# Optimization experiments

Hardware: AMD Instinct MI355X
Metric: run time of the kernel (lower is better)

Reference implementation:

```python
import jax, jax.numpy as jnp
import numpy as np

N, E = 20000, 320000
IN_CH, HID, NPRED = 64, 512, 12
NUM_GCN = 3   # num_gcn_layers=4 -> 1 + (4-2) layers
NUM_RNN = 2
BN_EPS = 1e-5


def setup_inputs() -> dict:
    key = jax.random.key(0)
    ks = jax.random.split(key, 16)
    s = 0.05  # init scale to keep activations sane
    return {
        "x": jax.random.normal(ks[0], (N, IN_CH), jnp.float32),
        "edge_index": jax.random.randint(ks[1], (2, E), 0, N, jnp.int32),
        "edge_weight": jax.random.uniform(ks[2], (E,), jnp.float32),
        "gcn0_W": jax.random.normal(ks[3], (IN_CH, HID), jnp.float32) * s,
        "gcn0_b": jnp.zeros((HID,), jnp.float32),
        "gcn_W": jax.random.normal(ks[4], (NUM_GCN - 1, HID, HID), jnp.float32) * s,
        "gcn_b": jnp.zeros((NUM_GCN - 1, HID), jnp.float32),
        "bn_gamma": jnp.ones((NUM_GCN, HID), jnp.float32),
        "bn_beta": jnp.zeros((NUM_GCN, HID), jnp.float32),
        "w_ih": jax.random.normal(ks[5], (NUM_RNN, HID, 4 * HID), jnp.float32) * s,
        "w_hh": jax.random.normal(ks[6], (NUM_RNN, HID, 4 * HID), jnp.float32) * s,
        "w_ch": jax.random.normal(ks[7], (NUM_RNN, HID, 3 * HID), jnp.float32) * s,
        "lstm_b": jnp.zeros((NUM_RNN, 4 * HID), jnp.float32),
        "out_W": jax.random.normal(ks[8], (HID, NPRED), jnp.float32) * s,
        "out_b": jnp.zeros((NPRED,), jnp.float32),
    }


def _gcn(x, W, b, src, dst, ew, n):
    h = x @ W                                   # [N, out]
    msg = ew[:, None] * h[src]                  # [E, out]
    return jax.ops.segment_sum(msg, dst, num_segments=n) + b


def _bn_relu(x, gamma, beta):
    mu = jnp.mean(x, axis=0)
    var = jnp.var(x, axis=0)
    return jax.nn.relu((x - mu) * jax.lax.rsqrt(var + BN_EPS) * gamma + beta)


def _peephole_cell(inp, h, c, Wih, Whh, Wch, b):
    H = h.shape[1]
    gates = inp @ Wih + h @ Whh + b             # [N, 4H]
    i_g, f_g, g_g, o_g = jnp.split(gates, 4, axis=1)
    g_g = g_g + c @ Wch[:, :H]
    i_g = jax.nn.sigmoid(i_g)
    f_g = jax.nn.sigmoid(f_g + c @ Wch[:, H:2 * H])
    g_g = jnp.tanh(g_g)
    cy = f_g * c + i_g * g_g
    o_g = o_g + cy @ Wch[:, 2 * H:]
    hy = jax.nn.sigmoid(o_g) * jnp.tanh(cy)
    return hy, cy


def reference(x, edge_index, edge_weight, gcn0_W, gcn0_b, gcn_W, gcn_b,
              bn_gamma, bn_beta, w_ih, w_hh, w_ch, lstm_b, out_W, out_b):
    src, dst = edge_index[0], edge_index[1]
    n = x.shape[0]
    # GCN stack: conv -> batchnorm (train-mode stats) -> relu (dropout=0)
    h = _gcn(x, gcn0_W, gcn0_b, src, dst, edge_weight, n)
    h = _bn_relu(h, bn_gamma[0], bn_beta[0])
    for i in range(NUM_GCN - 1):
        h = _gcn(h, gcn_W[i], gcn_b[i], src, dst, edge_weight, n)
        h = _bn_relu(h, bn_gamma[i + 1], bn_beta[i + 1])
    # seq_len == 1 after unsqueeze; cells chained sharing (h_t, c_t)
    h_t = jnp.zeros((n, HID), h.dtype)
    c_t = jnp.zeros((n, HID), h.dtype)
    for l in range(NUM_RNN):
        h_t, c_t = _peephole_cell(h, h_t, c_t, w_ih[l], w_hh[l], w_ch[l], lstm_b[l])
    out = h_t @ out_W + out_b                   # [N, num_predictions]
    return jnp.squeeze(out)
```

## Files before the change

kernel.cpp:

```cpp
#include <hip/hip_runtime.h>
#include <cstddef>

#define N_NODES 20000
#define N_EDGES 320000
#define IN_CH   64
#define HID     512
#define G4      2048
#define BN_EPS  1e-5f
#define F_OFF   0
#define G_OFF   512
#define I_OFF   1024
#define O_OFF   1536

typedef __attribute__((ext_vector_type(8))) __bf16 bf16x8;
typedef __attribute__((ext_vector_type(4))) float f32x4;

__device__ __forceinline__ float sigmoidf_(float x) {
  return 1.0f / (1.0f + expf(-x));
}

__device__ __forceinline__ unsigned short f2b(float f) {
  unsigned int u = __float_as_uint(f);
  u += 0x7FFFu + ((u >> 16) & 1u);
  return (unsigned short)(u >> 16);
}
__device__ __forceinline__ float b2f(unsigned short u) {
  return __uint_as_float(((unsigned int)u) << 16);
}

__device__ __forceinline__ void gld_lds16(const unsigned short* g, unsigned short* l) {
  __builtin_amdgcn_global_load_lds(
      (const __attribute__((address_space(1))) unsigned int*)(const void*)g,
      (__attribute__((address_space(3))) unsigned int*)(void*)l, 16, 0, 0);
}

__global__ __launch_bounds__(256) void zero_k(float* __restrict__ p, size_t n) {
  size_t i = ((size_t)blockIdx.x * 256 + threadIdx.x) * 4;
  if (i + 3 < n) {
    *(float4*)&p[i] = make_float4(0.f, 0.f, 0.f, 0.f);
  } else {
    for (; i < n; i++) p[i] = 0.f;
  }
}

struct TcvtDesc { const float* W; unsigned short* Wt; int K, NC, ldw, ldo; };
struct TcvtBatch { TcvtDesc d[18]; };

__global__ void tcvtb_k(TcvtBatch batch) {
  const TcvtDesc dd = batch.d[blockIdx.z];
  __shared__ float tile[32][33];
  const int n0 = blockIdx.x * 32, k0 = blockIdx.y * 32;
  if (n0 >= dd.NC || k0 >= dd.K) return;
  const int tx = threadIdx.x, ty = threadIdx.y;
  #pragma unroll
  for (int i = 0; i < 32; i += 8) {
    int k = k0 + ty + i, n = n0 + tx;
    tile[ty + i][tx] = (k < dd.K && n < dd.NC) ? dd.W[(size_t)k * dd.ldw + n] : 0.f;
  }
  __syncthreads();
  #pragma unroll
  for (int i = 0; i < 32; i += 8) {
    int n = n0 + ty + i, k = k0 + tx;
    if (n < dd.NC && k < dd.K) dd.Wt[(size_t)n * dd.ldo + k] = f2b(tile[tx][ty + i]);
  }
}

__global__ __launch_bounds__(256) void hist_k(const int* __restrict__ dst,
                                              int* __restrict__ counts) {
  int e = blockIdx.x * 256 + threadIdx.x;
  if (e < N_EDGES) atomicAdd(&counts[dst[e]], 1);
}

__global__ __launch_bounds__(1024) void scan_k(const int* __restrict__ counts,
                                               int* __restrict__ offsets,
                                               int* __restrict__ pos, int n) {
  __shared__ int tmp[1024];
  __shared__ int carry_s;
  const int tid = threadIdx.x;
  if (tid == 0) carry_s = 0;
  __syncthreads();
  for (int base = 0; base < n; base += 1024) {
    int i = base + tid;
    int v = (i < n) ? counts[i] : 0;
    tmp[tid] = v;
    __syncthreads();
    #pragma unroll
    for (int off = 1; off < 1024; off <<= 1) {
      int t = (tid >= off) ? tmp[tid - off] : 0;
      __syncthreads();
      tmp[tid] += t;
      __syncthreads();
    }
    if (i < n) {
      int excl = carry_s + tmp[tid] - v;
      offsets[i] = excl;
      pos[i] = excl;
    }
    __syncthreads();
    if (tid == 1023) carry_s += tmp[1023];
    __syncthreads();
  }
  if (tid == 0) offsets[n] = carry_s;
}

__global__ __launch_bounds__(256) void fill_k(
    const int* __restrict__ src, const int* __restrict__ dst,
    const float* __restrict__ ew, int* __restrict__ pos,
    int* __restrict__ s_s, float* __restrict__ w_s) {
  int e = blockIdx.x * 256 + threadIdx.x;
  if (e >= N_EDGES) return;
  int p = atomicAdd(&pos[dst[e]], 1);
  s_s[p] = src[e];
  w_s[p] = ew[e];
}

__global__ __launch_bounds__(64) void gather64_k(
    const float* __restrict__ x, const int* __restrict__ offsets,
    const int* __restrict__ s_s, const float* __restrict__ w_s,
    unsigned short* __restrict__ xg) {
  const int sub = threadIdx.x >> 4;
  const int cg  = threadIdx.x & 15;
  const int n   = blockIdx.x * 4 + sub;
  const int beg = offsets[n], end = offsets[n + 1];
  float4 acc = make_float4(0.f, 0.f, 0.f, 0.f);
  int i = beg;
  for (; i + 3 < end; i += 4) {
    const int   s0 = s_s[i],     s1 = s_s[i + 1];
    const int   s2 = s_s[i + 2], s3 = s_s[i + 3];
    const float w0 = w_s[i],     w1 = w_s[i + 1];
    const float w2 = w_s[i + 2], w3 = w_s[i + 3];
    const float4 v0 = *(const float4*)&x[(size_t)s0 * IN_CH + cg * 4];
    const float4 v1 = *(const float4*)&x[(size_t)s1 * IN_CH + cg * 4];
    const float4 v2 = *(const float4*)&x[(size_t)s2 * IN_CH + cg * 4];
    const float4 v3 = *(const float4*)&x[(size_t)s3 * IN_CH + cg * 4];
    acc.x = fmaf(w0, v0.x, acc.x); acc.y = fmaf(w0, v0.y, acc.y);
    acc.z = fmaf(w0, v0.z, acc.z); acc.w = fmaf(w0, v0.w, acc.w);
    acc.x = fmaf(w1, v1.x, acc.x); acc.y = fmaf(w1, v1.y, acc.y);
    acc.z = fmaf(w1, v1.z, acc.z); acc.w = fmaf(w1, v1.w, acc.w);
    acc.x = fmaf(w2, v2.x, acc.x); acc.y = fmaf(w2, v2.y, acc.y);
    acc.z = fmaf(w2, v2.z, acc.z); acc.w = fmaf(w2, v2.w, acc.w);
    acc.x = fmaf(w3, v3.x, acc.x); acc.y = fmaf(w3, v3.y, acc.y);
    acc.z = fmaf(w3, v3.z, acc.z); acc.w = fmaf(w3, v3.w, acc.w);
  }
  for (; i < end; i++) {
    const int   s = s_s[i];
    const float w = w_s[i];
    const float4 v = *(const float4*)&x[(size_t)s * IN_CH + cg * 4];
    acc.x = fmaf(w, v.x, acc.x);
    acc.y = fmaf(w, v.y, acc.y);
    acc.z = fmaf(w, v.z, acc.z);
    acc.w = fmaf(w, v.w, acc.w);
  }
  ushort4 o; o.x = f2b(acc.x); o.y = f2b(acc.y); o.z = f2b(acc.z); o.w = f2b(acc.w);
  *(ushort4*)&xg[(size_t)n * IN_CH + cg * 4] = o;
}

__global__ __launch_bounds__(128) void gather_k(
    const unsigned short* __restrict__ XW, const int* __restrict__ offsets,
    const int* __restrict__ s_s, const float* __restrict__ w_s,
    unsigned short* __restrict__ H) {
  const int n = blockIdx.x;
  const int t = threadIdx.x;
  const int beg = offsets[n], end = offsets[n + 1];
  float4 acc = make_float4(0.f, 0.f, 0.f, 0.f);
  int i = beg;
  for (; i + 3 < end; i += 4) {
    const int   s0 = s_s[i],     s1 = s_s[i + 1];
    const int   s2 = s_s[i + 2], s3 = s_s[i + 3];
    const float w0 = w_s[i],     w1 = w_s[i + 1];
    const float w2 = w_s[i + 2], w3 = w_s[i + 3];
    const ushort4 v0 = *(const ushort4*)&XW[(size_t)s0 * HID + t * 4];
    const ushort4 v1 = *(const ushort4*)&XW[(size_t)s1 * HID + t * 4];
    const ushort4 v2 = *(const ushort4*)&XW[(size_t)s2 * HID + t * 4];
    const ushort4 v3 = *(const ushort4*)&XW[(size_t)s3 * HID + t * 4];
    acc.x = fmaf(w0, b2f(v0.x), acc.x); acc.y = fmaf(w0, b2f(v0.y), acc.y);
    acc.z = fmaf(w0, b2f(v0.z), acc.z); acc.w = fmaf(w0, b2f(v0.w), acc.w);
    acc.x = fmaf(w1, b2f(v1.x), acc.x); acc.y = fmaf(w1, b2f(v1.y), acc.y);
    acc.z = fmaf(w1, b2f(v1.z), acc.z); acc.w = fmaf(w1, b2f(v1.w), acc.w);
    acc.x = fmaf(w2, b2f(v2.x), acc.x); acc.y = fmaf(w2, b2f(v2.y), acc.y);
    acc.z = fmaf(w2, b2f(v2.z), acc.z); acc.w = fmaf(w2, b2f(v2.w), acc.w);
    acc.x = fmaf(w3, b2f(v3.x), acc.x); acc.y = fmaf(w3, b2f(v3.y), acc.y);
    acc.z = fmaf(w3, b2f(v3.z), acc.z); acc.w = fmaf(w3, b2f(v3.w), acc.w);
  }
  for (; i < end; i++) {
    const int   s = s_s[i];
    const float w = w_s[i];
    const ushort4 v = *(const ushort4*)&XW[(size_t)s * HID + t * 4];
    acc.x = fmaf(w, b2f(v.x), acc.x);
    acc.y = fmaf(w, b2f(v.y), acc.y);
    acc.z = fmaf(w, b2f(v.z), acc.z);
    acc.w = fmaf(w, b2f(v.w), acc.w);
  }
  ushort4 o; o.x = f2b(acc.x); o.y = f2b(acc.y); o.z = f2b(acc.z); o.w = f2b(acc.w);
  *(ushort4*)&H[(size_t)n * HID + t * 4] = o;
}

__global__ __launch_bounds__(256) void bn_stats_k(
    const unsigned short* __restrict__ H, float* __restrict__ stats, int N)
{
  const int tx = threadIdx.x & 63;
  const int ty = threadIdx.x >> 6;
  const int col = blockIdx.x * 64 + tx;
  float s1 = 0.f, s2 = 0.f;
  for (int r = blockIdx.y * 4 + ty; r < N; r += gridDim.y * 4) {
    float v = b2f(H[(size_t)r * HID + col]);
    s1 += v; s2 += v * v;
  }
  __shared__ float red[2][4][64];
  red[0][ty][tx] = s1;
  red[1][ty][tx] = s2;
  __syncthreads();
  if (ty == 0) {
    s1 = red[0][0][tx] + red[0][1][tx] + red[0][2][tx] + red[0][3][tx];
    s2 = red[1][0][tx] + red[1][1][tx] + red[1][2][tx] + red[1][3][tx];
    atomicAdd(&stats[col], s1);
    atomicAdd(&stats[HID + col], s2);
  }
}

__global__ __launch_bounds__(256) void bn_apply_k(
    const unsigned short* __restrict__ H, const float* __restrict__ stats,
    const float* __restrict__ gamma, const float* __restrict__ beta,
    unsigned short* __restrict__ out, int N)
{
  size_t gid = (size_t)blockIdx.x * 256 + threadIdx.x;
  size_t idx = gid * 4;
  if (idx >= (size_t)N * HID) return;
  int col = (int)(idx & (HID - 1));
  const ushort4 v = *(const ushort4*)&H[idx];
  float r[4] = {b2f(v.x), b2f(v.y), b2f(v.z), b2f(v.w)};
  ushort4 o;
  unsigned short* op = &o.x;
  #pragma unroll
  for (int i = 0; i < 4; i++) {
    int c = col + i;
    float mean = stats[c] * (1.0f / N);
    float var  = stats[HID + c] * (1.0f / N) - mean * mean;
    float scale = gamma[c] / sqrtf(var + BN_EPS);
    float shift = beta[c] - mean * scale;
    op[i] = f2b(fmaxf(fmaf(r[i], scale, shift), 0.0f));
  }
  *(ushort4*)&out[idx] = o;
}

template<int BM, int BN>
__global__ __launch_bounds__(256) void gemm_bf16_k(
    const unsigned short* __restrict__ A, int lda,
    const unsigned short* __restrict__ A2, int lda2, int ksplit,
    const unsigned short* __restrict__ Bt,
    float* __restrict__ C, unsigned short* __restrict__ C16,
    const float* __restrict__ bias,
    int M, int K, int Ksmall, int NC, int ldc, int acc, int ntc,
    int nrowb, int ncolb)
{
  const int b   = blockIdx.x;
  const int xcd = b & 7;
  const int j   = b >> 3;
  const int col_b = j % ncolb;
  const int row_b = (j / ncolb) * 8 + xcd;
  if (row_b >= nrowb) return;

  constexpr int MI  = 2;
  constexpr int ASZ = BM * 64;
  constexpr int BSZ = BN * 64;
  __shared__ unsigned short As[2 * ASZ];
  __shared__ unsigned short Bs[2 * BSZ];
  const int row0 = row_b * BM;
  const int col0 = col_b * BN;
  const int Kthis = (col0 < 1024) ? K : Ksmall;
  const int t    = threadIdx.x;
  const int lane = t & 63;
  const int w    = t >> 6;
  const int wro  = (BN == 128) ? (w >> 1) * 32 : w * 32;
  const int wco  = (BN == 128) ? (w & 1) * 64 : 0;
  const int q    = lane >> 4;
  const int l16  = lane & 15;

  f32x4 accr[MI][4] = {};

  auto stage = [&](int buf, int k0) {
    unsigned short* Ad = As + buf * ASZ;
    unsigned short* Bd = Bs + buf * BSZ;
    #pragma unroll
    for (int i = 0; i < BM / 32; i++) {
      int s  = t + i * 256;
      int r  = s >> 3, cq = s & 7;
      int kq = (cq - r) & 7;
      int gr = row0 + r; if (gr > M - 1) gr = M - 1;
      int kk = k0 + kq * 8;
      const unsigned short* bp = (kk < ksplit) ? A : A2;
      size_t off = (kk < ksplit) ? ((size_t)gr * lda + kk)
                                 : ((size_t)gr * lda2 + (kk - ksplit));
      gld_lds16(bp + off, Ad + (size_t)s * 8);
    }
    #pragma unroll
    for (int i = 0; i < BN / 32; i++) {
      int s  = t + i * 256;
      int r  = s >> 3, cq = s & 7;
      int kq = (cq - r) & 7;
      gld_lds16(Bt + (size_t)(col0 + r) * K + k0 + kq * 8, Bd + (size_t)s * 8);
    }
  };

  stage(0, 0);
  int cur = 0;
  for (int k0 = 0; k0 < Kthis; k0 += 64) {
    __syncthreads();
    if (k0 + 64 < Kthis) stage(cur ^ 1, k0 + 64);

    const unsigned short* Ac = As + cur * ASZ;
    const unsigned short* Bc = Bs + cur * BSZ;
    #pragma unroll
    for (int ks = 0; ks < 2; ks++) {
      bf16x8 af[MI], bfr[4];
      #pragma unroll
      for (int mi = 0; mi < MI; mi++) {
        int r = wro + mi * 16 + l16;
        int slot = (ks * 4 + q + r) & 7;
        af[mi] = *(const bf16x8*)&Ac[r * 64 + slot * 8];
      }
      #pragma unroll
      for (int ni = 0; ni < 4; ni++) {
        int r = wco + ni * 16 + l16;
        int slot = (ks * 4 + q + r) & 7;
        bfr[ni] = *(const bf16x8*)&Bc[r * 64 + slot * 8];
      }
      #pragma unroll
      for (int mi = 0; mi < MI; mi++)
        #pragma unroll
        for (int ni = 0; ni < 4; ni++)
          accr[mi][ni] = __builtin_amdgcn_mfma_f32_16x16x32_bf16(
              af[mi], bfr[ni], accr[mi][ni], 0, 0, 0);
    }
    cur ^= 1;
  }

  #pragma unroll
  for (int mi = 0; mi < MI; mi++) {
    #pragma unroll
    for (int ni = 0; ni < 4; ni++) {
      int col = col0 + wco + ni * 16 + l16;
      #pragma unroll
      for (int r = 0; r < 4; r++) {
        int row = row0 + wro + mi * 16 + q * 4 + r;
        if (row < M) {
          float v = accr[mi][ni][r];
          if (C16) {
            C16[(size_t)row * ldc + col] = f2b(v);
          } else {
            float* cp = &C[(size_t)row * ldc + col];
            if (acc)       *cp += v;
            else if (bias) *cp  = v + bias[col];
            else if (ntc)  __builtin_nontemporal_store(v, cp);
            else           *cp  = v;
          }
        }
      }
    }
  }
}

__global__ __launch_bounds__(256) void cell1_k(
    const float* __restrict__ gates, const float* __restrict__ lb,
    const float* __restrict__ cin,
    float* __restrict__ cout, unsigned short* __restrict__ cout16, int ld16,
    int rows, int hasC)
{
  size_t gid = (size_t)blockIdx.x * 256 + threadIdx.x;
  if (gid >= (size_t)rows * HID) return;
  size_t row = gid >> 9;
  int    col = (int)(gid & (HID - 1));
  const float* g = &gates[row * G4];
  float ig = sigmoidf_(__builtin_nontemporal_load(&g[I_OFF + col]) + lb[col]);
  float gg = tanhf(__builtin_nontemporal_load(&g[G_OFF + col]) + lb[2 * HID + col]);
  float c;
  if (hasC) {
    float fg = sigmoidf_(__builtin_nontemporal_load(&g[F_OFF + col]) + lb[HID + col]);
    c = fg * cin[gid] + ig * gg;
  } else {
    c = ig * gg;
  }
  cout[gid] = c;
  cout16[row * ld16 + col] = f2b(c);
}

__global__ __launch_bounds__(256) void cell2_k(
    const float* __restrict__ gates, const float* __restrict__ obuf,
    const float* __restrict__ lb, const float* __restrict__ cy,
    unsigned short* __restrict__ hy16, int ld16, int rows)
{
  size_t gid = (size_t)blockIdx.x * 256 + threadIdx.x;
  if (gid >= (size_t)rows * HID) return;
  size_t row = gid >> 9;
  int    col = (int)(gid & (HID - 1));
  float ov = __builtin_nontemporal_load(&gates[row * G4 + O_OFF + col]);
  float og = sigmoidf_(ov + obuf[gid] + lb[3 * HID + col]);
  float h = og * tanhf(cy[gid]);
  hy16[row * ld16 + col] = f2b(h);
}

__global__ __launch_bounds__(256) void cellout_k(
    const float* __restrict__ gates, const float* __restrict__ obuf,
    const float* __restrict__ lb, const float* __restrict__ cy,
    const float* __restrict__ W, const float* __restrict__ b,
    float* __restrict__ out, int rows)
{
  int wave = (int)(((size_t)blockIdx.x * 256 + threadIdx.x) >> 6);
  int lane = threadIdx.x & 63;
  if (wave >= rows) return;
  const float* g  = &gates[(size_t)wave * G4 + O_OFF];
  const float* ob = &obuf[(size_t)wave * HID];
  const float* cr = &cy[(size_t)wave * HID];
  float hy[8];
  #pragma unroll
  for (int j = 0; j < 8; j++) {
    int k = lane + j * 64;
    float og = sigmoidf_(__builtin_nontemporal_load(&g[k]) + ob[k] + lb[3 * HID + k]);
    hy[j] = og * tanhf(cr[k]);
  }
  float acc[12] = {};
  #pragma unroll
  for (int j = 0; j < 8; j++) {
    int k = lane + j * 64;
    const float* wr = &W[k * 12];
    #pragma unroll
    for (int p = 0; p < 12; p++) acc[p] = fmaf(hy[j], wr[p], acc[p]);
  }
  #pragma unroll
  for (int p = 0; p < 12; p++) {
    float v = acc[p];
    #pragma unroll
    for (int off = 32; off > 0; off >>= 1) v += __shfl_down(v, off);
    if (lane == 0) out[(size_t)wave * 12 + p] = v + b[p];
  }
}

extern "C" void kernel_launch(void* const* d_in, const int* in_sizes, int n_in,
                              void* d_out, int out_size, void* d_ws, size_t ws_size,
                              hipStream_t stream) {
  const float* x     = (const float*)d_in[0];
  const int*   ei    = (const int*)d_in[1];
  const float* ew    = (const float*)d_in[2];
  const float* gcn0W = (const float*)d_in[3];
  const float* gcnW  = (const float*)d_in[5];
  const float* gamma = (const float*)d_in[7];
  const float* beta  = (const float*)d_in[8];
  const float* wih   = (const float*)d_in[9];
  const float* whh   = (const float*)d_in[10];
  const float* wch   = (const float*)d_in[11];
  const float* lstmb = (const float*)d_in[12];
  const float* outW  = (const float*)d_in[13];
  const float* outb  = (const float*)d_in[14];
  float* out = (float*)d_out;

  const int* src = ei;
  const int* dst = ei + N_EDGES;

  const int CH = (ws_size >= (size_t)215000000) ? 10000 : 5000;
  const int NCHUNK = N_NODES / CH;

  const size_t NH = (size_t)N_NODES * HID;
  float* ws = (float*)d_ws;
  float* gates = ws;
  float* bufH  = gates + (size_t)CH * G4;
  unsigned short* hbA16 = (unsigned short*)(bufH + NH);
  unsigned short* hbB16 = hbA16 + NH;
  unsigned short* x16   = hbB16 + NH;
  unsigned short* g0t   = x16 + (size_t)N_NODES * IN_CH;
  unsigned short* g1t   = g0t   + 512 * 64;
  unsigned short* g2t   = g1t   + 512 * 512;
  unsigned short* wih0t = g2t   + 512 * 512;
  unsigned short* wcat3 = wih0t + (size_t)1536 * 512;
  unsigned short* wch0ot= wcat3 + (size_t)2048 * 1536;
  unsigned short* wch1ot= wch0ot + 512 * 512;
  unsigned short* wend  = wch1ot + 512 * 512;
  unsigned short *a16, *tail16;
  if (CH == 5000) {
    a16  = hbB16;
    tail16 = wend;
  } else {
    a16  = wend;
    tail16 = a16 + (size_t)CH * 1024;
  }
  float* stats = (float*)tail16;
  int*   csr   = (int*)(stats + 3072);
  int*   counts  = csr;
  int*   offsets = csr + 20032;
  int*   cpos    = csr + 40064;
  int*   s_s     = csr + 60096;
  float* w_s     = (float*)(csr + 380096);

  unsigned short* bufH16 = (unsigned short*)bufH;
  float* cbuf = bufH;
  float* obuf = bufH + (size_t)CH * HID;

  const dim3 blk(256);
  auto gemm128 = [&](const unsigned short* A, int lda,
                     const unsigned short* A2, int lda2, int ksplit,
                     const unsigned short* Bt, float* C, unsigned short* C16,
                     const float* bias, int M, int K, int Ksmall, int NC, int ldc,
                     int acc) {
    int nrowb = (M + 63) / 64;
    int ncolb = NC / 128;
    int nblocks = 8 * ((nrowb + 7) / 8) * ncolb;
    hipLaunchKernelGGL((gemm_bf16_k<64, 128>), dim3(nblocks), blk, 0, stream,
                       A, lda, A2, lda2, ksplit, Bt, C, C16, bias,
                       M, K, Ksmall, NC, ldc, acc, 1, nrowb, ncolb);
  };
  auto gemm64 = [&](const unsigned short* A, int lda,
                    const unsigned short* Bt, float* C, unsigned short* C16,
                    const float* bias, int M, int K, int NC, int ldc, int acc) {
    int nrowb = (M + 127) / 128;
    int ncolb = NC / 64;
    int nblocks = 8 * ((nrowb + 7) / 8) * ncolb;
    hipLaunchKernelGGL((gemm_bf16_k<128, 64>), dim3(nblocks), blk, 0, stream,
                       A, lda, A, lda, K, Bt, C, C16, bias,
                       M, K, K, NC, ldc, acc, 0, nrowb, ncolb);
  };
  auto zero = [&](float* p, size_t n) {
    hipLaunchKernelGGL(zero_k, dim3((unsigned)((n / 4 + 255) / 256)), blk, 0, stream, p, n);
  };

  const float* wih1 = wih + (size_t)HID * G4;
  const float* whh1 = whh + (size_t)HID * G4;
  const float* wch1 = wch + (size_t)HID * 3 * HID;
  {
    TcvtBatch tb;
    int n = 0;
    auto add = [&](const float* W, unsigned short* Wt, int K, int NC, int ldw, int ldo) {
      tb.d[n++] = TcvtDesc{W, Wt, K, NC, ldw, ldo};
    };
    add(gcn0W, g0t, IN_CH, HID, HID, IN_CH);
    add(gcnW,                     g1t, HID, HID, HID, HID);
    add(gcnW + (size_t)HID * HID, g2t, HID, HID, HID, HID);
    add(wih + 2 * HID, wih0t,                      HID, HID, G4, HID);
    add(wih,           wih0t + (size_t)512 * 512,  HID, HID, G4, HID);
    add(wih + 3 * HID, wih0t + (size_t)1024 * 512, HID, HID, G4, HID);
    add(wih1 + HID,     wcat3 + (size_t)F_OFF * 1536,        HID, HID, G4, 1536);
    add(whh1 + HID,     wcat3 + (size_t)F_OFF * 1536 + 512,  HID, HID, G4, 1536);
    add(wch1 + HID,     wcat3 + (size_t)F_OFF * 1536 + 1024, HID, HID, 3 * HID, 1536);
    add(wih1 + 2 * HID, wcat3 + (size_t)G_OFF * 1536,        HID, HID, G4, 1536);
    add(whh1 + 2 * HID, wcat3 + (size_t)G_OFF * 1536 + 512,  HID, HID, G4, 1536);
    add(wch1,           wcat3 + (size_t)G_OFF * 1536 + 1024, HID, HID, 3 * HID, 1536);
    add(wih1,           wcat3 + (size_t)I_OFF * 1536,        HID, HID, G4, 1536);
    add(whh1,           wcat3 + (size_t)I_OFF * 1536 + 512,  HID, HID, G4, 1536);
    add(wih1 + 3 * HID, wcat3 + (size_t)O_OFF * 1536,        HID, HID, G4, 1536);
    add(whh1 + 3 * HID, wcat3 + (size_t)O_OFF * 1536 + 512,  HID, HID, G4, 1536);
    add(wch + 2 * HID,  wch0ot, HID, HID, 3 * HID, HID);
    add(wch1 + 2 * HID, wch1ot, HID, HID, 3 * HID, HID);
    hipLaunchKernelGGL(tcvtb_k, dim3(16, 16, 18), dim3(32, 8), 0, stream, tb);
  }

  const int e_blocks = (N_EDGES + 255) / 256;
  zero((float*)counts, N_NODES);
  zero(stats, 3 * 1024);
  hipLaunchKernelGGL(hist_k, dim3(e_blocks), blk, 0, stream, dst, counts);
  hipLaunchKernelGGL(scan_k, dim3(1), dim3(1024), 0, stream, counts, offsets, cpos, N_NODES);
  hipLaunchKernelGGL(fill_k, dim3(e_blocks), blk, 0, stream, src, dst, ew, cpos, s_s, w_s);

  hipLaunchKernelGGL(gather64_k, dim3(N_NODES / 4), dim3(64), 0, stream,
                     x, offsets, s_s, w_s, hbB16);
  gemm64(hbB16, IN_CH, g0t, nullptr, bufH16, nullptr, N_NODES, IN_CH, HID, HID, 0);
  hipLaunchKernelGGL(bn_stats_k, dim3(8, 64), blk, 0, stream, bufH16, stats, N_NODES);
  hipLaunchKernelGGL(bn_apply_k, dim3((unsigned)(NH / 4 / 256)), blk, 0, stream,
                     bufH16, stats, gamma, beta, hbA16, N_NODES);

  const unsigned short* gWt2[2] = {g1t, g2t};
  const unsigned short* gA2[2]  = {hbA16, hbB16};
  unsigned short*       gXW2[2] = {hbB16, hbA16};
  unsigned short*       gO2[2]  = {hbB16, hbA16};
  for (int l = 0; l < 2; l++) {
    gemm64(gA2[l], HID, gWt2[l], nullptr, gXW2[l], nullptr, N_NODES, HID, HID, HID, 0);
    hipLaunchKernelGGL(gather_k, dim3(N_NODES), dim3(128), 0, stream,
                       gXW2[l], offsets, s_s, w_s, bufH16);
    hipLaunchKernelGGL(bn_stats_k, dim3(8, 64), blk, 0, stream, bufH16,
                       stats + (l + 1) * 1024, N_NODES);
    hipLaunchKernelGGL(bn_apply_k, dim3((unsigned)(NH / 4 / 256)), blk, 0, stream,
                       bufH16, stats + (l + 1) * 1024, gamma + (l + 1) * HID,
                       beta + (l + 1) * HID, gO2[l], N_NODES);
  }
  unsigned short* hfin16 = hbA16;

  for (int ci = 0; ci < NCHUNK; ci++) {
    const int r0 = ci * CH;
    const unsigned short* h_c = hfin16 + (size_t)r0 * HID;
    const int cell_blocks = (int)(((size_t)CH * HID + 255) / 256);

    gemm128(h_c, HID, h_c, HID, HID, wih0t, gates + G_OFF, nullptr, nullptr,
            CH, HID, HID, 1536, G4, 0);
    hipLaunchKernelGGL(cell1_k, dim3(cell_blocks), blk, 0, stream,
                       gates, lstmb, (const float*)nullptr, cbuf, a16 + 512, 1024, CH, 0);
    gemm64(a16 + 512, 1024, wch0ot, obuf, nullptr, nullptr, CH, HID, HID, HID, 0);
    hipLaunchKernelGGL(cell2_k, dim3(cell_blocks), blk, 0, stream,
                       gates, obuf, lstmb, cbuf, a16, 1024, CH);

    gemm128(h_c, HID, a16, 1024, HID, wcat3, gates, nullptr, nullptr,
            CH, 1536, 1024, G4, G4, 0);
    hipLaunchKernelGGL(cell1_k, dim3(cell_blocks), blk, 0, stream,
                       gates, lstmb + G4, cbuf, cbuf, a16 + 512, 1024, CH, 1);
    gemm64(a16 + 512, 1024, wch1ot, obuf, nullptr, nullptr, CH, HID, HID, HID, 0);
    hipLaunchKernelGGL(cellout_k, dim3((CH * 64 + 255) / 256), blk, 0, stream,
                       gates, obuf, lstmb + G4, cbuf, outW, outb,
                       out + (size_t)r0 * 12, CH);
  }
}
```

Baseline: 873.4 us.

## Parallelize CSR scan and fuse BN statistics into the GCN gather

Replaces the single-block serial prefix scan with a two-pass multi-block scan (per-block scans, then per-block base offsets from block sums). Fuses the batchnorm column sum and sum-of-squares into the gather kernel, now a grid-stride kernel with per-thread accumulators and atomic adds at the end. It also folds the counts zeroing into the stats zero call, relying on counts being laid out directly after stats. This removes one full read of the hidden matrix per layer and the serial scan latency. In exchange it adds float atomics with nondeterministic summation order and fewer gather blocks.

```diff
diff --git a/kernel.cpp b/kernel.cpp
--- a/kernel.cpp
+++ b/kernel.cpp
@@ -71,36 +71,52 @@
   if (e < N_EDGES) atomicAdd(&counts[dst[e]], 1);
 }
 
-__global__ __launch_bounds__(1024) void scan_k(const int* __restrict__ counts,
+__global__ __launch_bounds__(128) void scan1_k(const int* __restrict__ counts,
                                                int* __restrict__ offsets,
-                                               int* __restrict__ pos, int n) {
-  __shared__ int tmp[1024];
-  __shared__ int carry_s;
-  const int tid = threadIdx.x;
-  if (tid == 0) carry_s = 0;
+                                               int* __restrict__ bsum, int n) {
+  __shared__ int sh[128];
+  const int b = blockIdx.x, t = threadIdx.x;
+  const int i = b * 128 + t;
+  const int v = (i < n) ? counts[i] : 0;
+  sh[t] = v;
   __syncthreads();
-  for (int base = 0; base < n; base += 1024) {
-    int i = base + tid;
-    int v = (i < n) ? counts[i] : 0;
-    tmp[tid] = v;
+  #pragma unroll
+  for (int off = 1; off < 128; off <<= 1) {
+    int u = (t >= off) ? sh[t - off] : 0;
     __syncthreads();
+    sh[t] += u;
+    __syncthreads();
+  }
+  if (i < n) offsets[i] = sh[t] - v;
+  if (t == 127) bsum[b] = sh[127];
+}
+
+__global__ __launch_bounds__(128) void scan2_k(const int* __restrict__ bsum,
+                                               int* __restrict__ offsets,
+                                               int* __restrict__ pos,
+                                               int n, int nb) {
+  __shared__ int red[128];
+  __shared__ int base_s;
+  const int b = blockIdx.x, t = threadIdx.x;
+  int part = 0;
+  if (t < b) part += bsum[t];
+  if (t + 128 < b) part += bsum[t + 128];
+  red[t] = part;
+  __syncthreads();
+  if (t < 64) {
+    int v = red[t] + red[t + 64];
     #pragma unroll
-    for (int off = 1; off < 1024; off <<= 1) {
-      int t = (tid >= off) ? tmp[tid - off] : 0;
-      __syncthreads();
-      tmp[tid] += t;
-      __syncthreads();
-    }
-    if (i < n) {
-      int excl = carry_s + tmp[tid] - v;
-      offsets[i] = excl;
-      pos[i] = excl;
-    }
-    __syncthreads();
-    if (tid == 1023) carry_s += tmp[1023];
-    __syncthreads();
-  }
-  if (tid == 0) offsets[n] = carry_s;
+    for (int off = 32; off > 0; off >>= 1) v += __shfl_down(v, off);
+    if (t == 0) base_s = v;
+  }
+  __syncthreads();
+  const int i = b * 128 + t;
+  if (i < n) {
+    int off = base_s + offsets[i];
+    offsets[i] = off;
+    pos[i] = off;
+  }
+  if (b == nb - 1 && t == 0) offsets[n] = base_s + bsum[b];
 }
 
 __global__ __launch_bounds__(256) void fill_k(
@@ -155,44 +171,58 @@
   *(ushort4*)&xg[(size_t)n * IN_CH + cg * 4] = o;
 }
 
-__global__ __launch_bounds__(128) void gather_k(
+__global__ __launch_bounds__(128) void gatherbn_k(
     const unsigned short* __restrict__ XW, const int* __restrict__ offsets,
     const int* __restrict__ s_s, const float* __restrict__ w_s,
-    unsigned short* __restrict__ H) {
-  const int n = blockIdx.x;
+    unsigned short* __restrict__ H, float* __restrict__ stats, int N) {
   const int t = threadIdx.x;
-  const int beg = offsets[n], end = offsets[n + 1];
-  float4 acc = make_float4(0.f, 0.f, 0.f, 0.f);
-  int i = beg;
-  for (; i + 3 < end; i += 4) {
-    const int   s0 = s_s[i],     s1 = s_s[i + 1];
-    const int   s2 = s_s[i + 2], s3 = s_s[i + 3];
-    const float w0 = w_s[i],     w1 = w_s[i + 1];
-    const float w2 = w_s[i + 2], w3 = w_s[i + 3];
-    const ushort4 v0 = *(const ushort4*)&XW[(size_t)s0 * HID + t * 4];
-    const ushort4 v1 = *(const ushort4*)&XW[(size_t)s1 * HID + t * 4];
-    const ushort4 v2 = *(const ushort4*)&XW[(size_t)s2 * HID + t * 4];
-    const ushort4 v3 = *(const ushort4*)&XW[(size_t)s3 * HID + t * 4];
-    acc.x = fmaf(w0, b2f(v0.x), acc.x); acc.y = fmaf(w0, b2f(v0.y), acc.y);
-    acc.z = fmaf(w0, b2f(v0.z), acc.z); acc.w = fmaf(w0, b2f(v0.w), acc.w);
-    acc.x = fmaf(w1, b2f(v1.x), acc.x); acc.y = fmaf(w1, b2f(v1.y), acc.y);
-    acc.z = fmaf(w1, b2f(v1.z), acc.z); acc.w = fmaf(w1, b2f(v1.w), acc.w);
-    acc.x = fmaf(w2, b2f(v2.x), acc.x); acc.y = fmaf(w2, b2f(v2.y), acc.y);
-    acc.z = fmaf(w2, b2f(v2.z), acc.z); acc.w = fmaf(w2, b2f(v2.w), acc.w);
-    acc.x = fmaf(w3, b2f(v3.x), acc.x); acc.y = fmaf(w3, b2f(v3.y), acc.y);
-    acc.z = fmaf(w3, b2f(v3.z), acc.z); acc.w = fmaf(w3, b2f(v3.w), acc.w);
-  }
-  for (; i < end; i++) {
-    const int   s = s_s[i];
-    const float w = w_s[i];
-    const ushort4 v = *(const ushort4*)&XW[(size_t)s * HID + t * 4];
-    acc.x = fmaf(w, b2f(v.x), acc.x);
-    acc.y = fmaf(w, b2f(v.y), acc.y);
-    acc.z = fmaf(w, b2f(v.z), acc.z);
-    acc.w = fmaf(w, b2f(v.w), acc.w);
-  }
-  ushort4 o; o.x = f2b(acc.x); o.y = f2b(acc.y); o.z = f2b(acc.z); o.w = f2b(acc.w);
-  *(ushort4*)&H[(size_t)n * HID + t * 4] = o;
+  float s1[4] = {0.f, 0.f, 0.f, 0.f};
+  float s2[4] = {0.f, 0.f, 0.f, 0.f};
+  for (int n = blockIdx.x; n < N; n += gridDim.x) {
+    const int beg = offsets[n], end = offsets[n + 1];
+    float4 acc = make_float4(0.f, 0.f, 0.f, 0.f);
+    int i = beg;
+    for (; i + 3 < end; i += 4) {
+      const int   e0 = s_s[i],     e1 = s_s[i + 1];
+      const int   e2 = s_s[i + 2], e3 = s_s[i + 3];
+      const float w0 = w_s[i],     w1 = w_s[i + 1];
+      const float w2 = w_s[i + 2], w3 = w_s[i + 3];
+      const ushort4 v0 = *(const ushort4*)&XW[(size_t)e0 * HID + t * 4];
+      const ushort4 v1 = *(const ushort4*)&XW[(size_t)e1 * HID + t * 4];
+      const ushort4 v2 = *(const ushort4*)&XW[(size_t)e2 * HID + t * 4];
+      const ushort4 v3 = *(const ushort4*)&XW[(size_t)e3 * HID + t * 4];
+      acc.x = fmaf(w0, b2f(v0.x), acc.x); acc.y = fmaf(w0, b2f(v0.y), acc.y);
+      acc.z = fmaf(w0, b2f(v0.z), acc.z); acc.w = fmaf(w0, b2f(v0.w), acc.w);
+      acc.x = fmaf(w1, b2f(v1.x), acc.x); acc.y = fmaf(w1, b2f(v1.y), acc.y);
+      acc.z = fmaf(w1, b2f(v1.z), acc.z); acc.w = fmaf(w1, b2f(v1.w), acc.w);
+      acc.x = fmaf(w2, b2f(v2.x), acc.x); acc.y = fmaf(w2, b2f(v2.y), acc.y);
+      acc.z = fmaf(w2, b2f(v2.z), acc.z); acc.w = fmaf(w2, b2f(v2.w), acc.w);
+      acc.x = fmaf(w3, b2f(v3.x), acc.x); acc.y = fmaf(w3, b2f(v3.y), acc.y);
+      acc.z = fmaf(w3, b2f(v3.z), acc.z); acc.w = fmaf(w3, b2f(v3.w), acc.w);
+    }
+    for (; i < end; i++) {
+      const int   s = s_s[i];
+      const float w = w_s[i];
+      const ushort4 v = *(const ushort4*)&XW[(size_t)s * HID + t * 4];
+      acc.x = fmaf(w, b2f(v.x), acc.x);
+      acc.y = fmaf(w, b2f(v.y), acc.y);
+      acc.z = fmaf(w, b2f(v.z), acc.z);
+      acc.w = fmaf(w, b2f(v.w), acc.w);
+    }
+    ushort4 o; o.x = f2b(acc.x); o.y = f2b(acc.y); o.z = f2b(acc.z); o.w = f2b(acc.w);
+    *(ushort4*)&H[(size_t)n * HID + t * 4] = o;
+    const float r0 = b2f(o.x), r1 = b2f(o.y), r2 = b2f(o.z), r3 = b2f(o.w);
+    s1[0] += r0; s2[0] += r0 * r0;
+    s1[1] += r1; s2[1] += r1 * r1;
+    s1[2] += r2; s2[2] += r2 * r2;
+    s1[3] += r3; s2[3] += r3 * r3;
+  }
+  const int col = t * 4;
+  #pragma unroll
+  for (int j = 0; j < 4; j++) {
+    atomicAdd(&stats[col + j], s1[j]);
+    atomicAdd(&stats[HID + col + j], s2[j]);
+  }
 }
 
 __global__ __launch_bounds__(256) void bn_stats_k(
@@ -489,6 +519,7 @@
   int*   cpos    = csr + 40064;
   int*   s_s     = csr + 60096;
   float* w_s     = (float*)(csr + 380096);
+  int*   bsum    = (int*)x16;
 
   unsigned short* bufH16 = (unsigned short*)bufH;
   float* cbuf = bufH;
@@ -552,10 +583,13 @@
   }
 
   const int e_blocks = (N_EDGES + 255) / 256;
-  zero((float*)counts, N_NODES);
-  zero(stats, 3 * 1024);
+  const int nscanb = (N_NODES + 127) / 128;
+  zero(stats, 3 * 1024 + N_NODES);
   hipLaunchKernelGGL(hist_k, dim3(e_blocks), blk, 0, stream, dst, counts);
-  hipLaunchKernelGGL(scan_k, dim3(1), dim3(1024), 0, stream, counts, offsets, cpos, N_NODES);
+  hipLaunchKernelGGL(scan1_k, dim3(nscanb), dim3(128), 0, stream,
+                     counts, offsets, bsum, N_NODES);
+  hipLaunchKernelGGL(scan2_k, dim3(nscanb), dim3(128), 0, stream,
+                     bsum, offsets, cpos, N_NODES, nscanb);
   hipLaunchKernelGGL(fill_k, dim3(e_blocks), blk, 0, stream, src, dst, ew, cpos, s_s, w_s);
 
   hipLaunchKernelGGL(gather64_k, dim3(N_NODES / 4), dim3(64), 0, stream,
@@ -571,9 +605,8 @@
   unsigned short*       gO2[2]  = {hbB16, hbA16};
   for (int l = 0; l < 2; l++) {
     gemm64(gA2[l], HID, gWt2[l], nullptr, gXW2[l], nullptr, N_NODES, HID, HID, HID, 0);
-    hipLaunchKernelGGL(gather_k, dim3(N_NODES), dim3(128), 0, stream,
-                       gXW2[l], offsets, s_s, w_s, bufH16);
-    hipLaunchKernelGGL(bn_stats_k, dim3(8, 64), blk, 0, stream, bufH16,
+    hipLaunchKernelGGL(gatherbn_k, dim3(2048), dim3(128), 0, stream,
+                       gXW2[l], offsets, s_s, w_s, bufH16,
                        stats + (l + 1) * 1024, N_NODES);
     hipLaunchKernelGGL(bn_apply_k, dim3((unsigned)(NH / 4 / 256)), blk, 0, stream,
                        bufH16, stats + (l + 1) * 1024, gamma + (l + 1) * HID,
```

Result: slower. 1.171 ms (+34.0%).
